# Performance work log

Hardware: AMD Instinct MI355X
Metric: run time of the kernel (lower is better)

The kernel has to match this reference:

```python
import jax, jax.numpy as jnp
import numpy as np

DIM = 256
NUM_HEADS = 8
WH, WW = 7, 7
N = WH * WW
B_ = 4096
TABLE = (2 * WH - 1) * (2 * WW - 1)  # 169


def _relative_position_index():
    ch, cw = np.meshgrid(np.arange(WH), np.arange(WW), indexing='ij')
    coords = np.stack([ch, cw]).reshape(2, -1)            # [2, N]
    rel = coords[:, :, None] - coords[:, None, :]          # [2, N, N]
    rel = rel.transpose(1, 2, 0)                           # [N, N, 2]
    rel[:, :, 0] += WH - 1
    rel[:, :, 1] += WW - 1
    rel[:, :, 0] *= 2 * WW - 1
    return jnp.asarray(rel.sum(-1), dtype=jnp.int32)       # [N, N]


def setup_inputs() -> dict:
    key = jax.random.key(0)
    ks = jax.random.split(key, 6)
    x = jax.random.normal(ks[0], (B_, N, DIM), dtype=jnp.float32)
    qkv_w = jax.random.normal(ks[1], (3 * DIM, DIM), dtype=jnp.float32) * 0.02
    qkv_b = jnp.zeros((3 * DIM,), dtype=jnp.float32)
    proj_w = jax.random.normal(ks[2], (DIM, DIM), dtype=jnp.float32) * 0.02
    proj_b = jnp.zeros((DIM,), dtype=jnp.float32)
    bias_table = jax.random.normal(ks[3], (TABLE, NUM_HEADS), dtype=jnp.float32) * 0.02
    rel_idx = _relative_position_index()
    return {"x": x, "qkv_w": qkv_w, "qkv_b": qkv_b, "proj_w": proj_w,
            "proj_b": proj_b, "bias_table": bias_table, "rel_idx": rel_idx}


def reference(x, qkv_w, qkv_b, proj_w, proj_b, bias_table, rel_idx):
    B, n, C = x.shape
    hd = C // NUM_HEADS
    scale = hd ** -0.5
    qkv = (jnp.einsum('bnc,oc->bno', x, qkv_w) + qkv_b)
    qkv = qkv.reshape(B, n, 3, NUM_HEADS, hd).transpose(2, 0, 3, 1, 4)
    q, k, v = qkv[0], qkv[1], qkv[2]
    attn = jnp.einsum('bhnd,bhmd->bhnm', q * scale, k)     # [B, H, N, N]
    # relative position bias gather: [N*N, H] -> [H, N, N]
    bias = bias_table[rel_idx.reshape(-1)].reshape(n, n, NUM_HEADS)
    attn = attn + bias.transpose(2, 0, 1)[None]
    attn = jax.nn.softmax(attn, axis=-1)
    out = jnp.einsum('bhnm,bhmd->bnhd', attn, v).reshape(B, n, C)
    out = jnp.einsum('bnc,oc->bno', out, proj_w) + proj_b
    return out
```

## Files before the change

### kernel.cpp

```cpp
#include <hip/hip_runtime.h>
#include <hip/hip_bf16.h>
#include <stdint.h>

#define NTOK 49
#define NH 8
#define NWIN 4096

typedef short bf16x8 __attribute__((ext_vector_type(8)));
typedef float f32x4 __attribute__((ext_vector_type(4)));

__device__ __forceinline__ f32x4 mfma16(bf16x8 a, bf16x8 b, f32x4 c) {
    return __builtin_amdgcn_mfma_f32_16x16x32_bf16(a, b, c, 0, 0, 0);
}
__device__ __forceinline__ bf16x8 ld8s(const unsigned short* p) {
    return *(const bf16x8*)p;
}
__device__ __forceinline__ unsigned int pk2bf(float a, float b) {
    __hip_bfloat162 h = __float22bfloat162_rn(float2{a, b});
    return *reinterpret_cast<unsigned int*>(&h);
}
__device__ __forceinline__ void st4bf(unsigned short* p, float a, float b, float c, float d) {
    uint2 u;
    u.x = pk2bf(a, b);
    u.y = pk2bf(c, d);
    *reinterpret_cast<uint2*>(p) = u;
}
__device__ __forceinline__ bf16x8 pk8(float4 f0, float4 f1) {
    union { bf16x8 v; unsigned int u[4]; } t;
    t.u[0] = pk2bf(f0.x, f0.y);
    t.u[1] = pk2bf(f0.z, f0.w);
    t.u[2] = pk2bf(f1.x, f1.y);
    t.u[3] = pk2bf(f1.z, f1.w);
    return t.v;
}
__device__ __forceinline__ unsigned short f2bf(float f) {
    union { float f; unsigned int u; } v; v.f = f;
    unsigned int r = v.u + 0x7FFFu + ((v.u >> 16) & 1u);
    return (unsigned short)(r >> 16);
}

__global__ void prep_kernel(const float* __restrict__ qkv_w,
                            const float* __restrict__ proj_w,
                            const float* __restrict__ bias_table,
                            const int* __restrict__ rel_idx,
                            unsigned short* __restrict__ wqkv,
                            unsigned short* __restrict__ wproj,
                            float* __restrict__ biasx)
{
    int i0 = blockIdx.x * blockDim.x + threadIdx.x;
    int stride = gridDim.x * blockDim.x;
    for (int t = i0; t < 768 * 256; t += stride) wqkv[t] = f2bf(qkv_w[t]);
    for (int t = i0; t < 256 * 256; t += stride) wproj[t] = f2bf(proj_w[t]);
    for (int t = i0; t < NH * 64 * 64; t += stride) {
        int h = t >> 12;
        int m = (t >> 6) & 63;
        int n = t & 63;
        float v;
        if (n >= NTOK)      v = -1e30f;
        else if (m >= NTOK) v = 0.0f;
        else                v = bias_table[rel_idx[m * NTOK + n] * NH + h];
        biasx[t] = v;
    }
}

__global__ __launch_bounds__(256, 2) void fused_kernel(
    const float* __restrict__ x,
    const float* __restrict__ qkv_b,
    const unsigned short* __restrict__ wqkv,
    const float* __restrict__ biasx,
    const unsigned short* __restrict__ wproj,
    const float* __restrict__ proj_b,
    float* __restrict__ out)
{
    __shared__ unsigned short smem[31744];
    unsigned short* ao = smem;
    unsigned short* qs = smem + 16896;
    unsigned short* ks = qs + 5120;
    unsigned short* vt = qs + 10240;
    unsigned short* Pb = qs;

    const int tid  = threadIdx.x;
    const int wave = tid >> 6;
    const int lane = tid & 63;
    const int l16  = lane & 15;
    const int lq   = lane >> 4;
    const int w    = blockIdx.x;
    const float scale = 0.17677669529663687f;

    const float* xw = x + (size_t)w * (NTOK * 256);
    bf16x8 afrag[4][8];
#pragma unroll
    for (int mt = 0; mt < 4; ++mt) {
        int tok = mt * 16 + l16;
#pragma unroll
        for (int c = 0; c < 8; ++c) {
            if (tok < NTOK) {
                const float* p = xw + tok * 256 + c * 32 + lq * 8;
                float4 f0 = *(const float4*)p;
                float4 f1 = *(const float4*)(p + 4);
                afrag[mt][c] = pk8(f0, f1);
            } else {
                union { bf16x8 v; unsigned int u[4]; } z;
                z.u[0] = z.u[1] = z.u[2] = z.u[3] = 0;
                afrag[mt][c] = z.v;
            }
        }
    }

    const int hl = wave >> 1;
    const int mh = wave & 1;

#pragma unroll 1
    for (int p = 0; p < 4; ++p) {
#pragma unroll
        for (int ti = 0; ti < 3; ++ti) {
            int tl   = wave * 3 + ti;
            int grp  = tl >> 2;
            int sub  = tl & 3;
            int tile = grp * 16 + p * 4 + sub;
            const unsigned short* bptr = wqkv + (size_t)(tile * 16 + l16) * 256 + lq * 8;
            bf16x8 bfr[8];
#pragma unroll
            for (int c = 0; c < 8; ++c) bfr[c] = ld8s(bptr + c * 32);

            f32x4 acc[4];
#pragma unroll
            for (int i = 0; i < 4; ++i) { f32x4 z = {0.f,0.f,0.f,0.f}; acc[i] = z; }

            if (grp < 2) {
#pragma unroll
                for (int c = 0; c < 8; ++c)
#pragma unroll
                    for (int nt = 0; nt < 4; ++nt)
                        acc[nt] = mfma16(bfr[c], afrag[nt][c], acc[nt]);
                int chb = tile * 16 + lq * 4;
                float4 bv = *(const float4*)(qkv_b + chb);
                int c0 = chb & 255;
                int hh = (c0 >> 5) & 1, d0 = c0 & 31;
                unsigned short* dst = (grp == 0 ? qs : ks) + (hh * 64) * 40 + d0;
                float sc = (grp == 0) ? scale : 1.0f;
#pragma unroll
                for (int nt = 0; nt < 4; ++nt) {
                    int tok = nt * 16 + l16;
                    st4bf(dst + tok * 40,
                          (acc[nt][0] + bv.x) * sc, (acc[nt][1] + bv.y) * sc,
                          (acc[nt][2] + bv.z) * sc, (acc[nt][3] + bv.w) * sc);
                }
            } else {
#pragma unroll
                for (int c = 0; c < 8; ++c)
#pragma unroll
                    for (int mt = 0; mt < 4; ++mt)
                        acc[mt] = mfma16(afrag[mt][c], bfr[c], acc[mt]);
                int ch = tile * 16 + l16;
                float bv = qkv_b[ch];
                int c0 = ch & 255;
                int hh = (c0 >> 5) & 1, d = c0 & 31;
                unsigned short* dst = vt + (hh * 32 + d) * 72;
#pragma unroll
                for (int mt = 0; mt < 4; ++mt) {
                    int tok0 = mt * 16 + lq * 4;
                    st4bf(dst + tok0, acc[mt][0] + bv, acc[mt][1] + bv,
                                      acc[mt][2] + bv, acc[mt][3] + bv);
                }
            }
        }
        __syncthreads();

        const int h = 2 * p + hl;
        bf16x8 kf[4], qf[2];
#pragma unroll
        for (int mt = 0; mt < 4; ++mt)
            kf[mt] = ld8s(&ks[(hl * 64 + mt * 16 + l16) * 40 + lq * 8]);
#pragma unroll
        for (int ni = 0; ni < 2; ++ni)
            qf[ni] = ld8s(&qs[(hl * 64 + mh * 32 + ni * 16 + l16) * 40 + lq * 8]);

        f32x4 se[4][2];
#pragma unroll
        for (int mt = 0; mt < 4; ++mt)
#pragma unroll
            for (int ni = 0; ni < 2; ++ni) { f32x4 z = {0.f,0.f,0.f,0.f}; se[mt][ni] = z; }
#pragma unroll
        for (int mt = 0; mt < 4; ++mt)
#pragma unroll
            for (int ni = 0; ni < 2; ++ni)
                se[mt][ni] = mfma16(kf[mt], qf[ni], se[mt][ni]);

        const float* bh = biasx + (h << 12);
        float rinv[2];
#pragma unroll
        for (int ni = 0; ni < 2; ++ni) {
            int q = mh * 32 + ni * 16 + l16;
            float lsum = 0.0f;
#pragma unroll
            for (int mt = 0; mt < 4; ++mt) {
                float4 bb = *(const float4*)(bh + q * 64 + mt * 16 + lq * 4);
                float e0 = __expf(se[mt][ni][0] + bb.x);
                float e1 = __expf(se[mt][ni][1] + bb.y);
                float e2 = __expf(se[mt][ni][2] + bb.z);
                float e3 = __expf(se[mt][ni][3] + bb.w);
                se[mt][ni][0] = e0; se[mt][ni][1] = e1;
                se[mt][ni][2] = e2; se[mt][ni][3] = e3;
                lsum += (e0 + e1) + (e2 + e3);
            }
            lsum += __shfl_xor(lsum, 16);
            lsum += __shfl_xor(lsum, 32);
            rinv[ni] = 1.0f / lsum;
        }
        __syncthreads();

#pragma unroll
        for (int ni = 0; ni < 2; ++ni) {
            int q = mh * 32 + ni * 16 + l16;
            float rv = rinv[ni];
#pragma unroll
            for (int mt = 0; mt < 4; ++mt)
                st4bf(&Pb[(hl * 64 + q) * 72 + mt * 16 + lq * 4],
                      se[mt][ni][0] * rv, se[mt][ni][1] * rv,
                      se[mt][ni][2] * rv, se[mt][ni][3] * rv);
        }
        __threadfence_block();

        bf16x8 vf[2][2], pf[2][2];
#pragma unroll
        for (int kc = 0; kc < 2; ++kc) {
#pragma unroll
            for (int mt = 0; mt < 2; ++mt)
                vf[mt][kc] = ld8s(&vt[(hl * 32 + mt * 16 + l16) * 72 + kc * 32 + lq * 8]);
#pragma unroll
            for (int ni = 0; ni < 2; ++ni)
                pf[ni][kc] = ld8s(&Pb[(hl * 64 + mh * 32 + ni * 16 + l16) * 72 + kc * 32 + lq * 8]);
        }
        f32x4 ot[2][2];
#pragma unroll
        for (int mt = 0; mt < 2; ++mt)
#pragma unroll
            for (int ni = 0; ni < 2; ++ni) { f32x4 z = {0.f,0.f,0.f,0.f}; ot[mt][ni] = z; }
#pragma unroll
        for (int kc = 0; kc < 2; ++kc)
#pragma unroll
            for (int mt = 0; mt < 2; ++mt)
#pragma unroll
                for (int ni = 0; ni < 2; ++ni)
                    ot[mt][ni] = mfma16(vf[mt][kc], pf[ni][kc], ot[mt][ni]);

#pragma unroll
        for (int mt = 0; mt < 2; ++mt)
#pragma unroll
            for (int ni = 0; ni < 2; ++ni) {
                int q = mh * 32 + ni * 16 + l16;
                st4bf(&ao[q * 264 + h * 32 + mt * 16 + lq * 4],
                      ot[mt][ni][0], ot[mt][ni][1], ot[mt][ni][2], ot[mt][ni][3]);
            }
        __syncthreads();
    }

    bf16x8 af2[4][8];
#pragma unroll
    for (int nt = 0; nt < 4; ++nt)
#pragma unroll
        for (int c = 0; c < 8; ++c)
            af2[nt][c] = ld8s(&ao[(nt * 16 + l16) * 264 + c * 32 + lq * 8]);

#pragma unroll
    for (int t4 = 0; t4 < 4; ++t4) {
        int tile = wave * 4 + t4;
        const unsigned short* wp = wproj + (size_t)(tile * 16 + l16) * 256 + lq * 8;
        bf16x8 wfr[8];
#pragma unroll
        for (int c = 0; c < 8; ++c) wfr[c] = ld8s(wp + c * 32);

        f32x4 acc[4];
#pragma unroll
        for (int i = 0; i < 4; ++i) { f32x4 z = {0.f,0.f,0.f,0.f}; acc[i] = z; }
#pragma unroll
        for (int c = 0; c < 8; ++c)
#pragma unroll
            for (int nt = 0; nt < 4; ++nt)
                acc[nt] = mfma16(wfr[c], af2[nt][c], acc[nt]);

        int chb = tile * 16 + lq * 4;
        float4 pb = *(const float4*)(proj_b + chb);
#pragma unroll
        for (int nt = 0; nt < 4; ++nt) {
            int tok = nt * 16 + l16;
            if (tok < NTOK) {
                float4 o;
                o.x = acc[nt][0] + pb.x;
                o.y = acc[nt][1] + pb.y;
                o.z = acc[nt][2] + pb.z;
                o.w = acc[nt][3] + pb.w;
                *(float4*)(out + ((size_t)w * NTOK + tok) * 256 + chb) = o;
            }
        }
    }
}

extern "C" void kernel_launch(void* const* d_in, const int* in_sizes, int n_in,
                              void* d_out, int out_size, void* d_ws, size_t ws_size,
                              hipStream_t stream) {
    const float* x          = (const float*)d_in[0];
    const float* qkv_w      = (const float*)d_in[1];
    const float* qkv_b      = (const float*)d_in[2];
    const float* proj_w     = (const float*)d_in[3];
    const float* proj_b     = (const float*)d_in[4];
    const float* bias_table = (const float*)d_in[5];
    const int*   rel_idx    = (const int*)d_in[6];
    float* out = (float*)d_out;

    char* ws = (char*)d_ws;
    unsigned short* wqkv  = (unsigned short*)ws;
    unsigned short* wproj = (unsigned short*)(ws + 393216);
    float*          biasx = (float*)(ws + 524288);

    prep_kernel<<<256, 256, 0, stream>>>(qkv_w, proj_w, bias_table, rel_idx,
                                         wqkv, wproj, biasx);
    fused_kernel<<<NWIN, 256, 0, stream>>>(x, qkv_b, wqkv, biasx, wproj,
                                           proj_b, out);
}
```

Measured before the change: 693.1 us.

## Use 8 waves per window and pass softmax probabilities to PV through lane shuffles

Doubles the block to 512 threads so each wave handles half the tokens in the QKV and projection GEMMs and one 16-query tile in attention. The x fragments are reloaded from global memory in every head-pair iteration, so they no longer stay resident in registers. The softmax probabilities are rearranged into MFMA operand layout with cross-lane shuffles, which removes the LDS round trip for P and one barrier. The aim is lower register pressure and higher occupancy, at the cost of four repeated x loads per window and extra shuffle instructions.

```diff
diff --git a/kernel.cpp b/kernel.cpp
--- a/kernel.cpp
+++ b/kernel.cpp
@@ -63,7 +63,7 @@
     }
 }
 
-__global__ __launch_bounds__(256, 2) void fused_kernel(
+__global__ __launch_bounds__(512, 4) void fused_kernel(
     const float* __restrict__ x,
     const float* __restrict__ qkv_b,
     const unsigned short* __restrict__ wqkv,
@@ -76,63 +76,64 @@
     unsigned short* ao = smem;
     unsigned short* qs = smem + 16896;
     unsigned short* ks = qs + 5120;
-    unsigned short* vt = qs + 10240;
-    unsigned short* Pb = qs;
+    unsigned short* vt = ks + 5120;
 
     const int tid  = threadIdx.x;
-    const int wave = tid >> 6;
+    const int wv   = tid >> 6;
     const int lane = tid & 63;
     const int l16  = lane & 15;
     const int lq   = lane >> 4;
     const int w    = blockIdx.x;
     const float scale = 0.17677669529663687f;
 
+    const int wh = wv & 1;
+    const int jt = wv >> 1;
+    const int hl = wv >> 2;
+    const int qt = wv & 3;
+
     const float* xw = x + (size_t)w * (NTOK * 256);
-    bf16x8 afrag[4][8];
-#pragma unroll
-    for (int mt = 0; mt < 4; ++mt) {
-        int tok = mt * 16 + l16;
-#pragma unroll
-        for (int c = 0; c < 8; ++c) {
-            if (tok < NTOK) {
-                const float* p = xw + tok * 256 + c * 32 + lq * 8;
-                float4 f0 = *(const float4*)p;
-                float4 f1 = *(const float4*)(p + 4);
-                afrag[mt][c] = pk8(f0, f1);
-            } else {
-                union { bf16x8 v; unsigned int u[4]; } z;
-                z.u[0] = z.u[1] = z.u[2] = z.u[3] = 0;
-                afrag[mt][c] = z.v;
-            }
-        }
-    }
-
-    const int hl = wave >> 1;
-    const int mh = wave & 1;
 
 #pragma unroll 1
     for (int p = 0; p < 4; ++p) {
+        bf16x8 xfr[2][8];
+#pragma unroll
+        for (int nt = 0; nt < 2; ++nt) {
+            int tok = wh * 32 + nt * 16 + l16;
+#pragma unroll
+            for (int c = 0; c < 8; ++c) {
+                if (tok < NTOK) {
+                    const float* pp = xw + tok * 256 + c * 32 + lq * 8;
+                    float4 f0 = *(const float4*)pp;
+                    float4 f1 = *(const float4*)(pp + 4);
+                    xfr[nt][c] = pk8(f0, f1);
+                } else {
+                    union { bf16x8 v; unsigned int u[4]; } z;
+                    z.u[0] = z.u[1] = z.u[2] = z.u[3] = 0;
+                    xfr[nt][c] = z.v;
+                }
+            }
+        }
+
 #pragma unroll
         for (int ti = 0; ti < 3; ++ti) {
-            int tl   = wave * 3 + ti;
-            int grp  = tl >> 2;
-            int sub  = tl & 3;
+            int tld  = jt * 3 + ti;
+            int grp  = tld >> 2;
+            int sub  = tld & 3;
             int tile = grp * 16 + p * 4 + sub;
             const unsigned short* bptr = wqkv + (size_t)(tile * 16 + l16) * 256 + lq * 8;
             bf16x8 bfr[8];
 #pragma unroll
             for (int c = 0; c < 8; ++c) bfr[c] = ld8s(bptr + c * 32);
 
-            f32x4 acc[4];
-#pragma unroll
-            for (int i = 0; i < 4; ++i) { f32x4 z = {0.f,0.f,0.f,0.f}; acc[i] = z; }
+            f32x4 acc[2];
+            { f32x4 z = {0.f,0.f,0.f,0.f}; acc[0] = z; acc[1] = z; }
 
             if (grp < 2) {
 #pragma unroll
                 for (int c = 0; c < 8; ++c)
 #pragma unroll
-                    for (int nt = 0; nt < 4; ++nt)
-                        acc[nt] = mfma16(bfr[c], afrag[nt][c], acc[nt]);
+                    for (int nt = 0; nt < 2; ++nt)
+                        acc[nt] = mfma16(bfr[c], xfr[nt][c], acc[nt]);
                 int chb = tile * 16 + lq * 4;
                 float4 bv = *(const float4*)(qkv_b + chb);
                 int c0 = chb & 255;
@@ -140,8 +141,8 @@
                 unsigned short* dst = (grp == 0 ? qs : ks) + (hh * 64) * 40 + d0;
                 float sc = (grp == 0) ? scale : 1.0f;
 #pragma unroll
-                for (int nt = 0; nt < 4; ++nt) {
-                    int tok = nt * 16 + l16;
+                for (int nt = 0; nt < 2; ++nt) {
+                    int tok = wh * 32 + nt * 16 + l16;
                     st4bf(dst + tok * 40,
                           (acc[nt][0] + bv.x) * sc, (acc[nt][1] + bv.y) * sc,
                           (acc[nt][2] + bv.z) * sc, (acc[nt][3] + bv.w) * sc);
@@ -150,141 +151,133 @@
 #pragma unroll
                 for (int c = 0; c < 8; ++c)
 #pragma unroll
-                    for (int mt = 0; mt < 4; ++mt)
-                        acc[mt] = mfma16(afrag[mt][c], bfr[c], acc[mt]);
+                    for (int nt = 0; nt < 2; ++nt)
+                        acc[nt] = mfma16(xfr[nt][c], bfr[c], acc[nt]);
                 int ch = tile * 16 + l16;
                 float bv = qkv_b[ch];
                 int c0 = ch & 255;
                 int hh = (c0 >> 5) & 1, d = c0 & 31;
                 unsigned short* dst = vt + (hh * 32 + d) * 72;
 #pragma unroll
-                for (int mt = 0; mt < 4; ++mt) {
-                    int tok0 = mt * 16 + lq * 4;
-                    st4bf(dst + tok0, acc[mt][0] + bv, acc[mt][1] + bv,
-                                      acc[mt][2] + bv, acc[mt][3] + bv);
+                for (int nt = 0; nt < 2; ++nt) {
+                    int tok0 = wh * 32 + nt * 16 + lq * 4;
+                    st4bf(dst + tok0, acc[nt][0] + bv, acc[nt][1] + bv,
+                                      acc[nt][2] + bv, acc[nt][3] + bv);
                 }
             }
         }
         __syncthreads();
 
         const int h = 2 * p + hl;
-        bf16x8 kf[4], qf[2];
+        bf16x8 kf[4];
 #pragma unroll
         for (int mt = 0; mt < 4; ++mt)
             kf[mt] = ld8s(&ks[(hl * 64 + mt * 16 + l16) * 40 + lq * 8]);
-#pragma unroll
-        for (int ni = 0; ni < 2; ++ni)
-            qf[ni] = ld8s(&qs[(hl * 64 + mh * 32 + ni * 16 + l16) * 40 + lq * 8]);
-
-        f32x4 se[4][2];
+        bf16x8 qf = ld8s(&qs[(hl * 64 + qt * 16 + l16) * 40 + lq * 8]);
+
+        f32x4 se[4];
+#pragma unroll
+        for (int mt = 0; mt < 4; ++mt) { f32x4 z = {0.f,0.f,0.f,0.f}; se[mt] = z; }
 #pragma unroll
         for (int mt = 0; mt < 4; ++mt)
-#pragma unroll
-            for (int ni = 0; ni < 2; ++ni) { f32x4 z = {0.f,0.f,0.f,0.f}; se[mt][ni] = z; }
-#pragma unroll
-        for (int mt = 0; mt < 4; ++mt)
-#pragma unroll
-            for (int ni = 0; ni < 2; ++ni)
-                se[mt][ni] = mfma16(kf[mt], qf[ni], se[mt][ni]);
-
+            se[mt] = mfma16(kf[mt], qf, se[mt]);
+
+        const int q = qt * 16 + l16;
         const float* bh = biasx + (h << 12);
-        float rinv[2];
-#pragma unroll
-        for (int ni = 0; ni < 2; ++ni) {
-            int q = mh * 32 + ni * 16 + l16;
-            float lsum = 0.0f;
-#pragma unroll
-            for (int mt = 0; mt < 4; ++mt) {
-                float4 bb = *(const float4*)(bh + q * 64 + mt * 16 + lq * 4);
-                float e0 = __expf(se[mt][ni][0] + bb.x);
-                float e1 = __expf(se[mt][ni][1] + bb.y);
-                float e2 = __expf(se[mt][ni][2] + bb.z);
-                float e3 = __expf(se[mt][ni][3] + bb.w);
-                se[mt][ni][0] = e0; se[mt][ni][1] = e1;
-                se[mt][ni][2] = e2; se[mt][ni][3] = e3;
-                lsum += (e0 + e1) + (e2 + e3);
-            }
-            lsum += __shfl_xor(lsum, 16);
-            lsum += __shfl_xor(lsum, 32);
-            rinv[ni] = 1.0f / lsum;
-        }
-        __syncthreads();
-
-#pragma unroll
-        for (int ni = 0; ni < 2; ++ni) {
-            int q = mh * 32 + ni * 16 + l16;
-            float rv = rinv[ni];
-#pragma unroll
-            for (int mt = 0; mt < 4; ++mt)
-                st4bf(&Pb[(hl * 64 + q) * 72 + mt * 16 + lq * 4],
-                      se[mt][ni][0] * rv, se[mt][ni][1] * rv,
-                      se[mt][ni][2] * rv, se[mt][ni][3] * rv);
-        }
-        __threadfence_block();
-
-        bf16x8 vf[2][2], pf[2][2];
+        float lsum = 0.0f;
+#pragma unroll
+        for (int mt = 0; mt < 4; ++mt) {
+            float4 bb = *(const float4*)(bh + q * 64 + mt * 16 + lq * 4);
+            float e0 = __expf(se[mt][0] + bb.x);
+            float e1 = __expf(se[mt][1] + bb.y);
+            float e2 = __expf(se[mt][2] + bb.z);
+            float e3 = __expf(se[mt][3] + bb.w);
+            se[mt][0] = e0; se[mt][1] = e1;
+            se[mt][2] = e2; se[mt][3] = e3;
+            lsum += (e0 + e1) + (e2 + e3);
+        }
+        lsum += __shfl_xor(lsum, 16);
+        lsum += __shfl_xor(lsum, 32);
+        float rv = 1.0f / lsum;
+
+        unsigned int P0[4], P1[4];
+#pragma unroll
+        for (int mt = 0; mt < 4; ++mt) {
+            P0[mt] = pk2bf(se[mt][0] * rv, se[mt][1] * rv);
+            P1[mt] = pk2bf(se[mt][2] * rv, se[mt][3] * rv);
+        }
+        int srcA = l16 + ((2 * lq) & 3) * 16;
+        int srcB = srcA + 16;
+        int hi = lq >> 1;
+        bf16x8 pf[2];
 #pragma unroll
         for (int kc = 0; kc < 2; ++kc) {
+            unsigned int a0 = (unsigned int)__shfl((int)P0[2 * kc],     srcA);
+            unsigned int a1 = (unsigned int)__shfl((int)P0[2 * kc + 1], srcA);
+            unsigned int b0 = (unsigned int)__shfl((int)P1[2 * kc],     srcA);
+            unsigned int b1 = (unsigned int)__shfl((int)P1[2 * kc + 1], srcA);
+            unsigned int c0 = (unsigned int)__shfl((int)P0[2 * kc],     srcB);
+            unsigned int c1 = (unsigned int)__shfl((int)P0[2 * kc + 1], srcB);
+            unsigned int d0 = (unsigned int)__shfl((int)P1[2 * kc],     srcB);
+            unsigned int d1 = (unsigned int)__shfl((int)P1[2 * kc + 1], srcB);
+            union { bf16x8 v; unsigned int u[4]; } t;
+            t.u[0] = hi ? a1 : a0;
+            t.u[1] = hi ? b1 : b0;
+            t.u[2] = hi ? c1 : c0;
+            t.u[3] = hi ? d1 : d0;
+            pf[kc] = t.v;
+        }
+
+        bf16x8 vf[2][2];
+#pragma unroll
+        for (int kc = 0; kc < 2; ++kc)
 #pragma unroll
             for (int mt = 0; mt < 2; ++mt)
                 vf[mt][kc] = ld8s(&vt[(hl * 32 + mt * 16 + l16) * 72 + kc * 32 + lq * 8]);
-#pragma unroll
-            for (int ni = 0; ni < 2; ++ni)
-                pf[ni][kc] = ld8s(&Pb[(hl * 64 + mh * 32 + ni * 16 + l16) * 72 + kc * 32 + lq * 8]);
-        }
-        f32x4 ot[2][2];
+
+        f32x4 ot[2];
+        { f32x4 z = {0.f,0.f,0.f,0.f}; ot[0] = z; ot[1] = z; }
+#pragma unroll
+        for (int kc = 0; kc < 2; ++kc)
+#pragma unroll
+            for (int mt = 0; mt < 2; ++mt)
+                ot[mt] = mfma16(vf[mt][kc], pf[kc], ot[mt]);
+
 #pragma unroll
         for (int mt = 0; mt < 2; ++mt)
-#pragma unroll
-            for (int ni = 0; ni < 2; ++ni) { f32x4 z = {0.f,0.f,0.f,0.f}; ot[mt][ni] = z; }
-#pragma unroll
-        for (int kc = 0; kc < 2; ++kc)
-#pragma unroll
-            for (int mt = 0; mt < 2; ++mt)
-#pragma unroll
-                for (int ni = 0; ni < 2; ++ni)
-                    ot[mt][ni] = mfma16(vf[mt][kc], pf[ni][kc], ot[mt][ni]);
-
-#pragma unroll
-        for (int mt = 0; mt < 2; ++mt)
-#pragma unroll
-            for (int ni = 0; ni < 2; ++ni) {
-                int q = mh * 32 + ni * 16 + l16;
-                st4bf(&ao[q * 264 + h * 32 + mt * 16 + lq * 4],
-                      ot[mt][ni][0], ot[mt][ni][1], ot[mt][ni][2], ot[mt][ni][3]);
-            }
+            st4bf(&ao[q * 264 + h * 32 + mt * 16 + lq * 4],
+                  ot[mt][0], ot[mt][1], ot[mt][2], ot[mt][3]);
         __syncthreads();
     }
 
-    bf16x8 af2[4][8];
-#pragma unroll
-    for (int nt = 0; nt < 4; ++nt)
+    bf16x8 af2[2][8];
+#pragma unroll
+    for (int nt = 0; nt < 2; ++nt)
 #pragma unroll
         for (int c = 0; c < 8; ++c)
-            af2[nt][c] = ld8s(&ao[(nt * 16 + l16) * 264 + c * 32 + lq * 8]);
+            af2[nt][c] = ld8s(&ao[(wh * 32 + nt * 16 + l16) * 264 + c * 32 + lq * 8]);
 
 #pragma unroll
     for (int t4 = 0; t4 < 4; ++t4) {
-        int tile = wave * 4 + t4;
+        int tile = jt * 4 + t4;
         const unsigned short* wp = wproj + (size_t)(tile * 16 + l16) * 256 + lq * 8;
         bf16x8 wfr[8];
 #pragma unroll
         for (int c = 0; c < 8; ++c) wfr[c] = ld8s(wp + c * 32);
 
-        f32x4 acc[4];
-#pragma unroll
-        for (int i = 0; i < 4; ++i) { f32x4 z = {0.f,0.f,0.f,0.f}; acc[i] = z; }
+        f32x4 acc[2];
+        { f32x4 z = {0.f,0.f,0.f,0.f}; acc[0] = z; acc[1] = z; }
 #pragma unroll
         for (int c = 0; c < 8; ++c)
 #pragma unroll
-            for (int nt = 0; nt < 4; ++nt)
+            for (int nt = 0; nt < 2; ++nt)
                 acc[nt] = mfma16(wfr[c], af2[nt][c], acc[nt]);
 
         int chb = tile * 16 + lq * 4;
         float4 pb = *(const float4*)(proj_b + chb);
 #pragma unroll
-        for (int nt = 0; nt < 4; ++nt) {
-            int tok = nt * 16 + l16;
+        for (int nt = 0; nt < 2; ++nt) {
+            int tok = wh * 32 + nt * 16 + l16;
             if (tok < NTOK) {
                 float4 o;
                 o.x = acc[nt][0] + pb.x;
@@ -316,6 +309,6 @@
 
     prep_kernel<<<256, 256, 0, stream>>>(qkv_w, proj_w, bias_table, rel_idx,
                                          wqkv, wproj, biasx);
-    fused_kernel<<<NWIN, 256, 0, stream>>>(x, qkv_b, wqkv, biasx, wproj,
+    fused_kernel<<<NWIN, 512, 0, stream>>>(x, qkv_b, wqkv, biasx, wproj,
                                            proj_b, out);
 }
```

Result: slower. 1.065 ms (+53.7%).
